# Optimization experiments

Measured on AMD Instinct MI355X. Metric: run time of the kernel, lower is better.

## Reference

```python
import jax, jax.numpy as jnp
import numpy as np

N_NODES = 100000
N_EDGES = 3200000
D_IN = 16
D_OUT = 32


def setup_inputs() -> dict:
    key = jax.random.key(0)
    ks = jax.random.split(key, 8)
    x = jax.random.normal(ks[0], (N_NODES, D_IN), dtype=jnp.float32)
    edge_index = jax.random.randint(ks[1], (2, N_EDGES), 0, N_NODES, dtype=jnp.int64)
    s = 1.0 / np.sqrt(D_IN)
    # mlp1: Linear(16,16) -> ReLU -> Linear(16,16)
    w1 = jax.random.uniform(ks[2], (D_IN, D_IN), jnp.float32, -s, s)
    b1 = jax.random.uniform(ks[3], (D_IN,), jnp.float32, -s, s)
    w2 = jax.random.uniform(ks[4], (D_IN, D_IN), jnp.float32, -s, s)
    b2 = jax.random.uniform(ks[5], (D_IN,), jnp.float32, -s, s)
    # SAGEConv(16,32): lin_l (neighbors, with bias), lin_r (root, no bias)
    wl = jax.random.uniform(ks[6], (D_IN, D_OUT), jnp.float32, -s, s)
    bl = jnp.zeros((D_OUT,), jnp.float32)
    wr = jax.random.uniform(ks[7], (D_IN, D_OUT), jnp.float32, -s, s)
    return {"x": x, "edge_index": edge_index, "w1": w1, "b1": b1,
            "w2": w2, "b2": b2, "wl": wl, "bl": bl, "wr": wr}


def reference(x, edge_index, w1, b1, w2, b2, wl, bl, wr):
    # MLP: Linear -> ReLU -> Linear
    h = jax.nn.relu(x @ w1 + b1) @ w2 + b2  # [N, 16]
    src, dst = edge_index[0], edge_index[1]
    # mean aggregation of neighbor (source) features at destination nodes
    msg = h[src]  # [E, 16]
    summed = jax.ops.segment_sum(msg, dst, num_segments=N_NODES)  # [N, 16]
    cnt = jax.ops.segment_sum(jnp.ones((msg.shape[0],), h.dtype), dst,
                              num_segments=N_NODES)
    mean = summed / jnp.maximum(cnt, 1.0)[:, None]
    # SAGEConv: lin_l(aggr) + lin_r(root)
    out = mean @ wl + bl + h @ wr  # [N, 32]
    return out
```

## Files before the change

### kernel.cpp

```cpp
#include <hip/hip_runtime.h>
#include <hip/hip_bf16.h>

#define N_NODES_C 100000
#define D_IN_C 16
#define D_OUT_C 32

__global__ __launch_bounds__(256) void mlp_kernel(
    const float* __restrict__ x,
    const float* __restrict__ w1, const float* __restrict__ b1,
    const float* __restrict__ w2, const float* __restrict__ b2,
    float* __restrict__ h, float* __restrict__ summed, int* __restrict__ cnt,
    int n_nodes) {
  __shared__ float sw1[256];
  __shared__ float sw2[256];
  __shared__ float sb1[16];
  __shared__ float sb2[16];
  int t = threadIdx.x;
  sw1[t] = w1[t];
  sw2[t] = w2[t];
  if (t < 16) { sb1[t] = b1[t]; sb2[t] = b2[t]; }
  __syncthreads();

  int n = blockIdx.x * blockDim.x + t;
  if (n >= n_nodes) return;

  float xi[16];
  const float4* xr = (const float4*)(x + (size_t)n * 16);
  float4 v0 = xr[0], v1 = xr[1], v2 = xr[2], v3 = xr[3];
  xi[0]=v0.x; xi[1]=v0.y; xi[2]=v0.z; xi[3]=v0.w;
  xi[4]=v1.x; xi[5]=v1.y; xi[6]=v1.z; xi[7]=v1.w;
  xi[8]=v2.x; xi[9]=v2.y; xi[10]=v2.z; xi[11]=v2.w;
  xi[12]=v3.x; xi[13]=v3.y; xi[14]=v3.z; xi[15]=v3.w;

  float t1[16];
#pragma unroll
  for (int j = 0; j < 16; ++j) {
    float acc = sb1[j];
#pragma unroll
    for (int k = 0; k < 16; ++k) acc += xi[k] * sw1[k * 16 + j];
    t1[j] = fmaxf(acc, 0.0f);
  }
  float hh[16];
#pragma unroll
  for (int j = 0; j < 16; ++j) {
    float acc = sb2[j];
#pragma unroll
    for (int k = 0; k < 16; ++k) acc += t1[k] * sw2[k * 16 + j];
    hh[j] = acc;
  }

  float4* hw = (float4*)(h + (size_t)n * 16);
  hw[0] = make_float4(hh[0], hh[1], hh[2], hh[3]);
  hw[1] = make_float4(hh[4], hh[5], hh[6], hh[7]);
  hw[2] = make_float4(hh[8], hh[9], hh[10], hh[11]);
  hw[3] = make_float4(hh[12], hh[13], hh[14], hh[15]);

  float4* sz = (float4*)(summed + (size_t)n * 16);
  float4 z = make_float4(0.f, 0.f, 0.f, 0.f);
  sz[0] = z; sz[1] = z; sz[2] = z; sz[3] = z;
  cnt[n] = 0;
}

__global__ __launch_bounds__(256) void scatter_kernel(
    const int* __restrict__ src, const int* __restrict__ dst,
    const float* __restrict__ h, float* __restrict__ summed,
    int* __restrict__ cnt, long long n_edges) {
  long long tid = (long long)blockIdx.x * blockDim.x + threadIdx.x;
  long long e = tid >> 4;
  int k = (int)(tid & 15);
  if (e >= n_edges) return;
  int s = src[e];
  int d = dst[e];
  float val = h[(size_t)s * 16 + k];
  atomicAdd(&summed[(size_t)d * 16 + k], val);
  if (k == 0) atomicAdd(&cnt[d], 1);
}

__global__ __launch_bounds__(256) void out_kernel(
    const float* __restrict__ h, const float* __restrict__ summed,
    const int* __restrict__ cnt,
    const float* __restrict__ wl, const float* __restrict__ bl,
    const float* __restrict__ wr, float* __restrict__ out, int n_nodes) {
  __shared__ float swl[512];
  __shared__ float swr[512];
  __shared__ float sbl[32];
  int t = threadIdx.x;
  for (int i = t; i < 512; i += 256) { swl[i] = wl[i]; swr[i] = wr[i]; }
  if (t < 32) sbl[t] = bl[t];
  __syncthreads();

  int gid = blockIdx.x * 256 + t;
  int n = gid >> 5;
  int j = gid & 31;
  if (n >= n_nodes) return;

  float inv = 1.0f / fmaxf((float)cnt[n], 1.0f);
  const float* hr = h + (size_t)n * 16;
  const float* sr = summed + (size_t)n * 16;
  float acc = sbl[j];
#pragma unroll
  for (int k = 0; k < 16; ++k) {
    acc += sr[k] * inv * swl[k * 32 + j] + hr[k] * swr[k * 32 + j];
  }
  out[(size_t)n * 32 + j] = acc;
}

extern "C" void kernel_launch(void* const* d_in, const int* in_sizes, int n_in,
                              void* d_out, int out_size, void* d_ws, size_t ws_size,
                              hipStream_t stream) {
  const float* x  = (const float*)d_in[0];
  const int* eidx = (const int*)d_in[1];
  const float* w1 = (const float*)d_in[2];
  const float* b1 = (const float*)d_in[3];
  const float* w2 = (const float*)d_in[4];
  const float* b2 = (const float*)d_in[5];
  const float* wl = (const float*)d_in[6];
  const float* bl = (const float*)d_in[7];
  const float* wr = (const float*)d_in[8];
  float* out = (float*)d_out;

  const int n_nodes = in_sizes[0] / D_IN_C;
  const long long n_edges = (long long)in_sizes[1] / 2;
  const int* src = eidx;
  const int* dst = eidx + n_edges;

  float* h      = (float*)d_ws;
  float* summed = h + (size_t)n_nodes * 16;
  int*   cnt    = (int*)(summed + (size_t)n_nodes * 16);

  {
    int blocks = (n_nodes + 255) / 256;
    mlp_kernel<<<blocks, 256, 0, stream>>>(x, w1, b1, w2, b2, h, summed, cnt, n_nodes);
  }
  {
    long long total = n_edges * 16;
    int blocks = (int)((total + 255) / 256);
    scatter_kernel<<<blocks, 256, 0, stream>>>(src, dst, h, summed, cnt, n_edges);
  }
  {
    long long total = (long long)n_nodes * 32;
    int blocks = (int)((total + 255) / 256);
    out_kernel<<<blocks, 256, 0, stream>>>(h, summed, cnt, wl, bl, wr, out, n_nodes);
  }
}
```

Before: 398.6 us.

## Replace float atomic scatter with CSR build and gather-based aggregation

```diff
diff --git a/kernel.cpp b/kernel.cpp
--- a/kernel.cpp
+++ b/kernel.cpp
@@ -4,12 +4,13 @@
 #define N_NODES_C 100000
 #define D_IN_C 16
 #define D_OUT_C 32
+#define SCAN_CHUNK 2048
 
 __global__ __launch_bounds__(256) void mlp_kernel(
     const float* __restrict__ x,
     const float* __restrict__ w1, const float* __restrict__ b1,
     const float* __restrict__ w2, const float* __restrict__ b2,
-    float* __restrict__ h, float* __restrict__ summed, int* __restrict__ cnt,
+    float* __restrict__ h, int* __restrict__ cnt, int* __restrict__ pos,
     int n_nodes) {
   __shared__ float sw1[256];
   __shared__ float sw2[256];
@@ -55,30 +56,92 @@
   hw[2] = make_float4(hh[8], hh[9], hh[10], hh[11]);
   hw[3] = make_float4(hh[12], hh[13], hh[14], hh[15]);
 
-  float4* sz = (float4*)(summed + (size_t)n * 16);
-  float4 z = make_float4(0.f, 0.f, 0.f, 0.f);
-  sz[0] = z; sz[1] = z; sz[2] = z; sz[3] = z;
   cnt[n] = 0;
-}
-
-__global__ __launch_bounds__(256) void scatter_kernel(
+  pos[n] = 0;
+}
+
+__global__ __launch_bounds__(256) void hist_kernel(
+    const int* __restrict__ dst, int* __restrict__ cnt, int n_edges) {
+  int e = blockIdx.x * 256 + threadIdx.x;
+  if (e >= n_edges) return;
+  atomicAdd(&cnt[dst[e]], 1);
+}
+
+__global__ __launch_bounds__(256) void scanA_kernel(
+    const int* __restrict__ cnt, int* __restrict__ bsums, int n) {
+  __shared__ int sdata[256];
+  int b = blockIdx.x, t = threadIdx.x;
+  int base = b * SCAN_CHUNK + t * 8;
+  int s = 0;
+#pragma unroll
+  for (int i = 0; i < 8; ++i) {
+    int idx = base + i;
+    if (idx < n) s += cnt[idx];
+  }
+  sdata[t] = s;
+  __syncthreads();
+  for (int off = 128; off > 0; off >>= 1) {
+    if (t < off) sdata[t] += sdata[t + off];
+    __syncthreads();
+  }
+  if (t == 0) bsums[b] = sdata[0];
+}
+
+__global__ void scanB_kernel(int* __restrict__ bsums, int nb) {
+  if (threadIdx.x == 0 && blockIdx.x == 0) {
+    int run = 0;
+    for (int i = 0; i < nb; ++i) { int v = bsums[i]; bsums[i] = run; run += v; }
+  }
+}
+
+__global__ __launch_bounds__(256) void scanC_kernel(
+    const int* __restrict__ cnt, const int* __restrict__ bsums,
+    int* __restrict__ row_ptr, int n) {
+  __shared__ int sdata[256];
+  int b = blockIdx.x, t = threadIdx.x;
+  int base = b * SCAN_CHUNK + t * 8;
+  int vals[8];
+  int s = 0;
+#pragma unroll
+  for (int i = 0; i < 8; ++i) {
+    int idx = base + i;
+    int v = (idx < n) ? cnt[idx] : 0;
+    vals[i] = v;
+    s += v;
+  }
+  sdata[t] = s;
+  __syncthreads();
+  for (int off = 1; off < 256; off <<= 1) {
+    int y = (t >= off) ? sdata[t - off] : 0;
+    __syncthreads();
+    sdata[t] += y;
+    __syncthreads();
+  }
+  int excl = sdata[t] - s;
+  int running = bsums[b] + excl;
+#pragma unroll
+  for (int i = 0; i < 8; ++i) {
+    int idx = base + i;
+    if (idx < n) row_ptr[idx] = running;
+    running += vals[i];
+  }
+}
+
+__global__ __launch_bounds__(256) void place_kernel(
     const int* __restrict__ src, const int* __restrict__ dst,
-    const float* __restrict__ h, float* __restrict__ summed,
-    int* __restrict__ cnt, long long n_edges) {
-  long long tid = (long long)blockIdx.x * blockDim.x + threadIdx.x;
-  long long e = tid >> 4;
-  int k = (int)(tid & 15);
+    const int* __restrict__ row_ptr, int* __restrict__ pos,
+    int* __restrict__ src_sorted, int n_edges) {
+  int e = blockIdx.x * 256 + threadIdx.x;
   if (e >= n_edges) return;
   int s = src[e];
   int d = dst[e];
-  float val = h[(size_t)s * 16 + k];
-  atomicAdd(&summed[(size_t)d * 16 + k], val);
-  if (k == 0) atomicAdd(&cnt[d], 1);
-}
-
-__global__ __launch_bounds__(256) void out_kernel(
-    const float* __restrict__ h, const float* __restrict__ summed,
-    const int* __restrict__ cnt,
+  int idx = row_ptr[d] + atomicAdd(&pos[d], 1);
+  src_sorted[idx] = s;
+}
+
+__global__ __launch_bounds__(256) void aggregate_kernel(
+    const float* __restrict__ h, const int* __restrict__ src_sorted,
+    const int* __restrict__ row_ptr, const int* __restrict__ cnt,
     const float* __restrict__ wl, const float* __restrict__ bl,
     const float* __restrict__ wr, float* __restrict__ out, int n_nodes) {
   __shared__ float swl[512];
@@ -89,20 +152,36 @@
   if (t < 32) sbl[t] = bl[t];
   __syncthreads();
 
-  int gid = blockIdx.x * 256 + t;
-  int n = gid >> 5;
-  int j = gid & 31;
+  int wave = t >> 6;
+  int lane = t & 63;
+  int n = blockIdx.x * 4 + wave;
   if (n >= n_nodes) return;
 
-  float inv = 1.0f / fmaxf((float)cnt[n], 1.0f);
-  const float* hr = h + (size_t)n * 16;
-  const float* sr = summed + (size_t)n * 16;
-  float acc = sbl[j];
-#pragma unroll
-  for (int k = 0; k < 16; ++k) {
-    acc += sr[k] * inv * swl[k * 32 + j] + hr[k] * swr[k * 32 + j];
-  }
-  out[(size_t)n * 32 + j] = acc;
+  int sub = lane >> 4;
+  int k = lane & 15;
+
+  int base = row_ptr[n];
+  int deg = cnt[n];
+
+  float acc = 0.0f;
+  for (int e = sub; e < deg; e += 4) {
+    int s = src_sorted[base + e];
+    acc += h[(size_t)s * 16 + k];
+  }
+  acc += __shfl_xor(acc, 16, 64);
+  acc += __shfl_xor(acc, 32, 64);
+  float mean = acc / fmaxf((float)deg, 1.0f);
+  float hval = h[(size_t)n * 16 + k];
+
+  int j = lane & 31;
+  float o = sbl[j];
+#pragma unroll
+  for (int kk = 0; kk < 16; ++kk) {
+    float m = __shfl(mean, kk, 64);
+    float hv = __shfl(hval, kk, 64);
+    o += m * swl[kk * 32 + j] + hv * swr[kk * 32 + j];
+  }
+  if (lane < 32) out[(size_t)n * 32 + j] = o;
 }
 
 extern "C" void kernel_launch(void* const* d_in, const int* in_sizes, int n_in,
@@ -120,26 +199,27 @@
   float* out = (float*)d_out;
 
   const int n_nodes = in_sizes[0] / D_IN_C;
-  const long long n_edges = (long long)in_sizes[1] / 2;
+  const int n_edges = in_sizes[1] / 2;
   const int* src = eidx;
   const int* dst = eidx + n_edges;
 
-  float* h      = (float*)d_ws;
-  float* summed = h + (size_t)n_nodes * 16;
-  int*   cnt    = (int*)(summed + (size_t)n_nodes * 16);
-
-  {
-    int blocks = (n_nodes + 255) / 256;
-    mlp_kernel<<<blocks, 256, 0, stream>>>(x, w1, b1, w2, b2, h, summed, cnt, n_nodes);
-  }
-  {
-    long long total = n_edges * 16;
-    int blocks = (int)((total + 255) / 256);
-    scatter_kernel<<<blocks, 256, 0, stream>>>(src, dst, h, summed, cnt, n_edges);
-  }
-  {
-    long long total = (long long)n_nodes * 32;
-    int blocks = (int)((total + 255) / 256);
-    out_kernel<<<blocks, 256, 0, stream>>>(h, summed, cnt, wl, bl, wr, out, n_nodes);
-  }
-}
+  float* h        = (float*)d_ws;
+  int* cnt        = (int*)(h + (size_t)n_nodes * 16);
+  int* pos        = cnt + n_nodes;
+  int* row_ptr    = pos + n_nodes;
+  int* bsums      = row_ptr + n_nodes;
+  int* src_sorted = bsums + 256;
+
+  const int nb_scan = (n_nodes + SCAN_CHUNK - 1) / SCAN_CHUNK;
+
+  mlp_kernel<<<(n_nodes + 255) / 256, 256, 0, stream>>>(
+      x, w1, b1, w2, b2, h, cnt, pos, n_nodes);
+  hist_kernel<<<(n_edges + 255) / 256, 256, 0, stream>>>(dst, cnt, n_edges);
+  scanA_kernel<<<nb_scan, 256, 0, stream>>>(cnt, bsums, n_nodes);
+  scanB_kernel<<<1, 64, 0, stream>>>(bsums, nb_scan);
+  scanC_kernel<<<nb_scan, 256, 0, stream>>>(cnt, bsums, row_ptr, n_nodes);
+  place_kernel<<<(n_edges + 255) / 256, 256, 0, stream>>>(
+      src, dst, row_ptr, pos, src_sorted, n_edges);
+  aggregate_kernel<<<(n_nodes + 3) / 4, 256, 0, stream>>>(
+      h, src_sorted, row_ptr, cnt, wl, bl, wr, out, n_nodes);
+}
```

Measured after the change: 554.5 us. 1.39x slower.

## Bucket edges by destination and accumulate neighbor sums in shared memory

Applied to the files above, without the earlier changes.

```diff
diff --git a/kernel.cpp b/kernel.cpp
--- a/kernel.cpp
+++ b/kernel.cpp
@@ -1,21 +1,25 @@
 #include <hip/hip_runtime.h>
 #include <hip/hip_bf16.h>
 
-#define N_NODES_C 100000
 #define D_IN_C 16
-#define D_OUT_C 32
+#define BUCKET_SHIFT 9
+#define BUCKET_NODES 512
+#define CAP 18432
+#define PT 16
+#define PART_CHUNK 4096
 
 __global__ __launch_bounds__(256) void mlp_kernel(
     const float* __restrict__ x,
     const float* __restrict__ w1, const float* __restrict__ b1,
     const float* __restrict__ w2, const float* __restrict__ b2,
-    float* __restrict__ h, float* __restrict__ summed, int* __restrict__ cnt,
+    float* __restrict__ h, int* __restrict__ bcur,
     int n_nodes) {
   __shared__ float sw1[256];
   __shared__ float sw2[256];
   __shared__ float sb1[16];
   __shared__ float sb2[16];
   int t = threadIdx.x;
+  if (blockIdx.x == 0) bcur[t] = 0;
   sw1[t] = w1[t];
   sw2[t] = w2[t];
   if (t < 16) { sb1[t] = b1[t]; sb2[t] = b2[t]; }
@@ -54,33 +58,114 @@
   hw[1] = make_float4(hh[4], hh[5], hh[6], hh[7]);
   hw[2] = make_float4(hh[8], hh[9], hh[10], hh[11]);
   hw[3] = make_float4(hh[12], hh[13], hh[14], hh[15]);
-
-  float4* sz = (float4*)(summed + (size_t)n * 16);
-  float4 z = make_float4(0.f, 0.f, 0.f, 0.f);
-  sz[0] = z; sz[1] = z; sz[2] = z; sz[3] = z;
-  cnt[n] = 0;
-}
-
-__global__ __launch_bounds__(256) void scatter_kernel(
+}
+
+__global__ __launch_bounds__(256) void part_kernel(
     const int* __restrict__ src, const int* __restrict__ dst,
-    const float* __restrict__ h, float* __restrict__ summed,
-    int* __restrict__ cnt, long long n_edges) {
-  long long tid = (long long)blockIdx.x * blockDim.x + threadIdx.x;
-  long long e = tid >> 4;
-  int k = (int)(tid & 15);
-  if (e >= n_edges) return;
-  int s = src[e];
-  int d = dst[e];
-  float val = h[(size_t)s * 16 + k];
-  atomicAdd(&summed[(size_t)d * 16 + k], val);
-  if (k == 0) atomicAdd(&cnt[d], 1);
+    int* __restrict__ bcur, int* __restrict__ part,
+    int* __restrict__ cnt, int nbuck, int n_edges) {
+  __shared__ int lhist[256];
+  __shared__ int lofs[256];
+  int t = threadIdx.x;
+  int base = blockIdx.x * PART_CHUNK;
+
+  int zi = blockIdx.x * 256 + t;
+  if (zi < nbuck * BUCKET_NODES) cnt[zi] = 0;
+
+  if (t < nbuck) lhist[t] = 0;
+  __syncthreads();
+
+  int d[PT], s[PT];
+#pragma unroll
+  for (int i = 0; i < PT; ++i) {
+    int e = base + i * 256 + t;
+    if (e < n_edges) { d[i] = dst[e]; s[i] = src[e]; }
+    else d[i] = -1;
+  }
+#pragma unroll
+  for (int i = 0; i < PT; ++i) {
+    if (d[i] >= 0) atomicAdd(&lhist[d[i] >> BUCKET_SHIFT], 1);
+  }
+  __syncthreads();
+  if (t < nbuck) {
+    int c = lhist[t];
+    int r = (c > 0) ? atomicAdd(&bcur[t], c) : 0;
+    lofs[t] = t * CAP + r;
+  }
+  __syncthreads();
+#pragma unroll
+  for (int i = 0; i < PT; ++i) {
+    if (d[i] >= 0) {
+      int b = d[i] >> BUCKET_SHIFT;
+      int p = atomicAdd(&lofs[b], 1);
+      part[p] = ((d[i] & (BUCKET_NODES - 1)) << 17) | s[i];
+    }
+  }
+}
+
+__global__ __launch_bounds__(256) void acc_kernel(
+    const float* __restrict__ h, const int* __restrict__ part,
+    const int* __restrict__ bcur, int* __restrict__ cnt,
+    float* __restrict__ partial,
+    int nbuck, int C) {
+  __shared__ float acc[BUCKET_NODES * 16];
+  __shared__ int dcnt[BUCKET_NODES];
+  int t = threadIdx.x;
+  int b = blockIdx.x / C;
+  int c = blockIdx.x % C;
+
+#pragma unroll
+  for (int i = t; i < BUCKET_NODES * 16; i += 256) acc[i] = 0.0f;
+  if (t < 256) { dcnt[t] = 0; dcnt[t + 256] = 0; }
+  __syncthreads();
+
+  int count = bcur[b];
+  int start = b * CAP + (int)((long long)count * c / C);
+  int end   = b * CAP + (int)((long long)count * (c + 1) / C);
+
+  int g = t >> 4;
+  int k = t & 15;
+
+  for (int it = start; it < end; it += 128) {
+    int pk[8]; float v[8];
+#pragma unroll
+    for (int u = 0; u < 8; ++u) {
+      int e = it + u * 16 + g;
+      pk[u] = (e < end) ? part[e] : -1;
+    }
+#pragma unroll
+    for (int u = 0; u < 8; ++u) {
+      v[u] = (pk[u] >= 0) ? h[(size_t)(pk[u] & 0x1FFFF) * 16 + k] : 0.0f;
+    }
+#pragma unroll
+    for (int u = 0; u < 8; ++u) {
+      if (pk[u] >= 0) {
+        int dl = pk[u] >> 17;
+        atomicAdd(&acc[dl * 16 + k], v[u]);
+        if (k == 0) atomicAdd(&dcnt[dl], 1);
+      }
+    }
+  }
+  __syncthreads();
+
+  float* pout = partial + (size_t)c * nbuck * BUCKET_NODES * 16
+                        + (size_t)b * BUCKET_NODES * 16;
+#pragma unroll
+  for (int i = t; i < BUCKET_NODES * 16; i += 256) pout[i] = acc[i];
+  if (t < 256) {
+    int n0 = b * BUCKET_NODES + t;
+    int n1 = n0 + 256;
+    if (dcnt[t]) atomicAdd(&cnt[n0], dcnt[t]);
+    if (dcnt[t + 256]) atomicAdd(&cnt[n1], dcnt[t + 256]);
+  }
 }
 
 __global__ __launch_bounds__(256) void out_kernel(
-    const float* __restrict__ h, const float* __restrict__ summed,
+    const float* __restrict__ h, const float* __restrict__ partial,
     const int* __restrict__ cnt,
     const float* __restrict__ wl, const float* __restrict__ bl,
-    const float* __restrict__ wr, float* __restrict__ out, int n_nodes) {
+    const float* __restrict__ wr, float* __restrict__ out,
+    int n_nodes, int nbuck, int C) {
   __shared__ float swl[512];
   __shared__ float swr[512];
   __shared__ float sbl[32];
@@ -89,20 +174,47 @@
   if (t < 32) sbl[t] = bl[t];
   __syncthreads();
 
-  int gid = blockIdx.x * 256 + t;
-  int n = gid >> 5;
-  int j = gid & 31;
+  int n = blockIdx.x * 256 + t;
   if (n >= n_nodes) return;
 
+  size_t stride = (size_t)nbuck * BUCKET_NODES * 16;
+  float mean[16];
+#pragma unroll
+  for (int k = 0; k < 16; ++k) mean[k] = 0.0f;
+  for (int c = 0; c < C; ++c) {
+    const float4* pr = (const float4*)(partial + c * stride + (size_t)n * 16);
+    float4 p0 = pr[0], p1 = pr[1], p2 = pr[2], p3 = pr[3];
+    mean[0]+=p0.x; mean[1]+=p0.y; mean[2]+=p0.z; mean[3]+=p0.w;
+    mean[4]+=p1.x; mean[5]+=p1.y; mean[6]+=p1.z; mean[7]+=p1.w;
+    mean[8]+=p2.x; mean[9]+=p2.y; mean[10]+=p2.z; mean[11]+=p2.w;
+    mean[12]+=p3.x; mean[13]+=p3.y; mean[14]+=p3.z; mean[15]+=p3.w;
+  }
   float inv = 1.0f / fmaxf((float)cnt[n], 1.0f);
-  const float* hr = h + (size_t)n * 16;
-  const float* sr = summed + (size_t)n * 16;
-  float acc = sbl[j];
+#pragma unroll
+  for (int k = 0; k < 16; ++k) mean[k] *= inv;
+
+  float hr[16];
+  const float4* hp = (const float4*)(h + (size_t)n * 16);
+  float4 h0 = hp[0], h1 = hp[1], h2 = hp[2], h3 = hp[3];
+  hr[0]=h0.x; hr[1]=h0.y; hr[2]=h0.z; hr[3]=h0.w;
+  hr[4]=h1.x; hr[5]=h1.y; hr[6]=h1.z; hr[7]=h1.w;
+  hr[8]=h2.x; hr[9]=h2.y; hr[10]=h2.z; hr[11]=h2.w;
+  hr[12]=h3.x; hr[13]=h3.y; hr[14]=h3.z; hr[15]=h3.w;
+
+  float o[32];
+#pragma unroll
+  for (int j = 0; j < 32; ++j) o[j] = sbl[j];
 #pragma unroll
   for (int k = 0; k < 16; ++k) {
-    acc += sr[k] * inv * swl[k * 32 + j] + hr[k] * swr[k * 32 + j];
-  }
-  out[(size_t)n * 32 + j] = acc;
+#pragma unroll
+    for (int j = 0; j < 32; ++j) {
+      o[j] += mean[k] * swl[k * 32 + j] + hr[k] * swr[k * 32 + j];
+    }
+  }
+  float4* ow = (float4*)(out + (size_t)n * 32);
+#pragma unroll
+  for (int q = 0; q < 8; ++q)
+    ow[q] = make_float4(o[q*4], o[q*4+1], o[q*4+2], o[q*4+3]);
 }
 
 extern "C" void kernel_launch(void* const* d_in, const int* in_sizes, int n_in,
@@ -120,26 +232,29 @@
   float* out = (float*)d_out;
 
   const int n_nodes = in_sizes[0] / D_IN_C;
-  const long long n_edges = (long long)in_sizes[1] / 2;
+  const int n_edges = in_sizes[1] / 2;
   const int* src = eidx;
   const int* dst = eidx + n_edges;
 
-  float* h      = (float*)d_ws;
-  float* summed = h + (size_t)n_nodes * 16;
-  int*   cnt    = (int*)(summed + (size_t)n_nodes * 16);
-
-  {
-    int blocks = (n_nodes + 255) / 256;
-    mlp_kernel<<<blocks, 256, 0, stream>>>(x, w1, b1, w2, b2, h, summed, cnt, n_nodes);
-  }
-  {
-    long long total = n_edges * 16;
-    int blocks = (int)((total + 255) / 256);
-    scatter_kernel<<<blocks, 256, 0, stream>>>(src, dst, h, summed, cnt, n_edges);
-  }
-  {
-    long long total = (long long)n_nodes * 32;
-    int blocks = (int)((total + 255) / 256);
-    out_kernel<<<blocks, 256, 0, stream>>>(h, summed, cnt, wl, bl, wr, out, n_nodes);
-  }
-}
+  const int nbuck = (n_nodes + BUCKET_NODES - 1) / BUCKET_NODES;
+
+  float* h     = (float*)d_ws;
+  int* part    = (int*)(h + (size_t)n_nodes * 16);
+  int* bcur    = part + (size_t)nbuck * CAP;
+  int* cnt     = bcur + 256;
+  float* partial = (float*)(cnt + (size_t)nbuck * BUCKET_NODES);
+
+  size_t fixed = (size_t)n_nodes * 16 * 4 + (size_t)nbuck * CAP * 4
+               + 256 * 4 + (size_t)nbuck * BUCKET_NODES * 4;
+  size_t per_copy = (size_t)nbuck * BUCKET_NODES * 16 * 4;
+  int C = (ws_size >= fixed + 4 * per_copy) ? 4 : 2;
+
+  mlp_kernel<<<(n_nodes + 255) / 256, 256, 0, stream>>>(
+      x, w1, b1, w2, b2, h, bcur, n_nodes);
+  part_kernel<<<(n_edges + PART_CHUNK - 1) / PART_CHUNK, 256, 0, stream>>>(
+      src, dst, bcur, part, cnt, nbuck, n_edges);
+  acc_kernel<<<nbuck * C, 256, 0, stream>>>(
+      h, part, bcur, cnt, partial, nbuck, C);
+  out_kernel<<<(n_nodes + 255) / 256, 256, 0, stream>>>(
+      h, partial, cnt, wl, bl, wr, out, n_nodes, nbuck, C);
+}
```

New measurement: 479.5 us. 20.3% more time.
